# Kernel tuning notes

Measured on AMD Instinct MI355X. Metric: run time of the kernel, lower is better.

Reference implementation:

```python
import jax, jax.numpy as jnp
import numpy as np

EPS = 1e-5

def _layernorm(x, gamma, beta):
    # LayerNormalization over last axis (channels), epsilon=1e-5
    mu = jnp.mean(x, axis=-1, keepdims=True)
    var = jnp.var(x, axis=-1, keepdims=True)
    return (x - mu) * jax.lax.rsqrt(var + EPS) * gamma + beta

def setup_inputs() -> dict:
    key = jax.random.key(0)
    ks = jax.random.split(key, 6)
    B, H, W, C = 8, 64, 64, 256
    std = 0.1  # NIN init_scale
    return {
        "x": jax.random.normal(ks[0], (B, H, W, C), dtype=jnp.float32),
        "ln_gamma": jnp.ones((C,), dtype=jnp.float32),
        "ln_beta": jnp.zeros((C,), dtype=jnp.float32),
        "wq": jax.random.normal(ks[1], (C, C), dtype=jnp.float32) * std,
        "bq": jnp.zeros((C,), dtype=jnp.float32),
        "wk": jax.random.normal(ks[2], (C, C), dtype=jnp.float32) * std,
        "bk": jnp.zeros((C,), dtype=jnp.float32),
        "wv": jax.random.normal(ks[3], (C, C), dtype=jnp.float32) * std,
        "bv": jnp.zeros((C,), dtype=jnp.float32),
        "wo": jax.random.normal(ks[4], (C, C), dtype=jnp.float32) * std,
        "bo": jnp.zeros((C,), dtype=jnp.float32),
    }

def reference(x, ln_gamma, ln_beta, wq, bq, wk, bk, wv, bv, wo, bo):
    B, H, W, C = x.shape
    h = _layernorm(x, ln_gamma, ln_beta)
    # 1x1 convs == per-pixel channel matmuls
    q = jnp.einsum('bhwc,cd->bhwd', h, wq) + bq
    k = jnp.einsum('bhwc,cd->bhwd', h, wk) + bk
    v = jnp.einsum('bhwc,cd->bhwd', h, wv) + bv
    scale = jnp.float32(C) ** -0.5
    # dense spatial attention over all H*W tokens
    w = jnp.einsum('bhwc,bijc->bhwij', q, k) * scale  # [B,H,W,H,W]
    w = jax.nn.softmax(w.reshape(B, H, W, H * W), axis=-1).reshape(B, H, W, H, W)
    h = jnp.einsum('bhwij,bijc->bhwc', w, v)
    h = jnp.einsum('bhwc,cd->bhwd', h, wo) + bo
    return x + h
```

## Files before the change

### kernel.cpp

```cpp
#include <hip/hip_runtime.h>
#include <stdint.h>

#define NB    8
#define NTOK  4096
#define TOK   32768
#define CDIM  256
#define BQ    128
#define BK    64
#define NT    (NTOK / BK)

#define KPITCH 264
#define VPITCH 68
#define KTILE_SH (BK * KPITCH)
#define VTILE_SH (CDIM * VPITCH)
#define KCH   33
#define VCH   34
#define TOTCH (KCH + VCH)

typedef __attribute__((ext_vector_type(8))) short bf16x8;
typedef __attribute__((ext_vector_type(4))) float f32x4;

#define SSCALE 0.09016844f

static __device__ __forceinline__ unsigned short f2bf(float f) {
    union { float f; unsigned u; } v; v.f = f;
    unsigned r = v.u + 0x7fffu + ((v.u >> 16) & 1u);
    return (unsigned short)(r >> 16);
}

static __device__ __forceinline__ void dma16(const unsigned short* g, unsigned short* l) {
    __builtin_amdgcn_global_load_lds(
        (const __attribute__((address_space(1))) unsigned int*)g,
        (__attribute__((address_space(3))) unsigned int*)l,
        16, 0, 0);
}

__global__ __launch_bounds__(256) void prep_kernel(
        const float* __restrict__ x,
        const float* __restrict__ gamma,
        const float* __restrict__ beta,
        const float* __restrict__ w0, const float* __restrict__ w1,
        const float* __restrict__ w2, const float* __restrict__ w3,
        unsigned short* __restrict__ h_bf,
        unsigned short* __restrict__ wt) {
    int bx = blockIdx.x;
    if (bx >= TOK / 4) {
        int id = bx - TOK / 4;
        int m = id >> 8, dd = id & 255;
        const float* src = (m == 0) ? w0 : (m == 1) ? w1 : (m == 2) ? w2 : w3;
        wt[m * (CDIM * CDIM) + dd * CDIM + threadIdx.x] = f2bf(src[threadIdx.x * CDIM + dd]);
        return;
    }
    int w = threadIdx.x >> 6;
    int lane = threadIdx.x & 63;
    int token = bx * 4 + w;
    const float4 xv = ((const float4*)(x + (size_t)token * CDIM))[lane];
    float s = xv.x + xv.y + xv.z + xv.w;
    #pragma unroll
    for (int off = 1; off < 64; off <<= 1) s += __shfl_xor(s, off, 64);
    float mean = s * (1.0f / 256.0f);
    float d0 = xv.x - mean, d1 = xv.y - mean, d2 = xv.z - mean, d3 = xv.w - mean;
    float ss = d0 * d0 + d1 * d1 + d2 * d2 + d3 * d3;
    #pragma unroll
    for (int off = 1; off < 64; off <<= 1) ss += __shfl_xor(ss, off, 64);
    float rstd = rsqrtf(ss * (1.0f / 256.0f) + 1e-5f);
    float4 g = ((const float4*)gamma)[lane];
    float4 b = ((const float4*)beta)[lane];
    ushort4 o;
    o.x = f2bf(d0 * rstd * g.x + b.x);
    o.y = f2bf(d1 * rstd * g.y + b.y);
    o.z = f2bf(d2 * rstd * g.z + b.z);
    o.w = f2bf(d3 * rstd * g.w + b.w);
    ((ushort4*)(h_bf + (size_t)token * CDIM))[lane] = o;
}

__global__ __launch_bounds__(128) void qkv_kernel(
        const unsigned short* __restrict__ h_bf,
        const unsigned short* __restrict__ wts,
        const float* __restrict__ bq,
        const float* __restrict__ bk,
        const float* __restrict__ bv,
        unsigned short* __restrict__ q_bf,
        unsigned short* __restrict__ k2,
        unsigned short* __restrict__ vt2) {
    __shared__ unsigned short VT[64][VPITCH];
    int tid = threadIdx.x;
    int w = tid >> 6, lane = tid & 63, quad = lane >> 4, l16 = lane & 15;
    int blk = blockIdx.x;
    int gy = blockIdx.y;
    int nt0 = gy * 4;
    int tok_base = blk * 64 + w * 32;

    bf16x8 afr[2][8];
    #pragma unroll
    for (int s = 0; s < 2; ++s)
        #pragma unroll
        for (int kk = 0; kk < 8; ++kk)
            afr[s][kk] = *(const bf16x8*)(h_bf + (size_t)(tok_base + s * 16 + l16) * CDIM + kk * 32 + quad * 8);

    {
        const unsigned short* wq_t = wts;
        #pragma unroll
        for (int ntl = 0; ntl < 4; ++ntl) {
            int nt = nt0 + ntl;
            f32x4 acc0 = {0.f, 0.f, 0.f, 0.f};
            f32x4 acc1 = {0.f, 0.f, 0.f, 0.f};
            #pragma unroll
            for (int kk = 0; kk < 8; ++kk) {
                bf16x8 bfr = *(const bf16x8*)(wq_t + (size_t)(nt * 16 + l16) * CDIM + kk * 32 + quad * 8);
                acc0 = __builtin_amdgcn_mfma_f32_16x16x32_bf16(afr[0][kk], bfr, acc0, 0, 0, 0);
                acc1 = __builtin_amdgcn_mfma_f32_16x16x32_bf16(afr[1][kk], bfr, acc1, 0, 0, 0);
            }
            int d = nt * 16 + l16;
            float bb = bq[d];
            #pragma unroll
            for (int r = 0; r < 4; ++r) {
                q_bf[(size_t)(tok_base + quad * 4 + r) * CDIM + d]      = f2bf((acc0[r] + bb) * SSCALE);
                q_bf[(size_t)(tok_base + 16 + quad * 4 + r) * CDIM + d] = f2bf((acc1[r] + bb) * SSCALE);
            }
        }
    }
    {
        const unsigned short* wk_t = wts + CDIM * CDIM;
        unsigned short* kdst = k2 + (size_t)blk * KTILE_SH;
        int row0 = w * 32 + quad * 4;
        #pragma unroll
        for (int ntl = 0; ntl < 4; ++ntl) {
            int nt = nt0 + ntl;
            f32x4 acc0 = {0.f, 0.f, 0.f, 0.f};
            f32x4 acc1 = {0.f, 0.f, 0.f, 0.f};
            #pragma unroll
            for (int kk = 0; kk < 8; ++kk) {
                bf16x8 bfr = *(const bf16x8*)(wk_t + (size_t)(nt * 16 + l16) * CDIM + kk * 32 + quad * 8);
                acc0 = __builtin_amdgcn_mfma_f32_16x16x32_bf16(afr[0][kk], bfr, acc0, 0, 0, 0);
                acc1 = __builtin_amdgcn_mfma_f32_16x16x32_bf16(afr[1][kk], bfr, acc1, 0, 0, 0);
            }
            int d = nt * 16 + l16;
            float bb = bk[d];
            #pragma unroll
            for (int r = 0; r < 4; ++r) {
                kdst[(size_t)(row0 + r) * KPITCH + d]      = f2bf(acc0[r] + bb);
                kdst[(size_t)(row0 + 16 + r) * KPITCH + d] = f2bf(acc1[r] + bb);
            }
        }
    }
    {
        const unsigned short* wv_t = wts + 2 * CDIM * CDIM;
        int col0 = w * 32 + quad * 4;
        #pragma unroll
        for (int ntl = 0; ntl < 4; ++ntl) {
            int nt = nt0 + ntl;
            f32x4 acc0 = {0.f, 0.f, 0.f, 0.f};
            f32x4 acc1 = {0.f, 0.f, 0.f, 0.f};
            #pragma unroll
            for (int kk = 0; kk < 8; ++kk) {
                bf16x8 bfr = *(const bf16x8*)(wv_t + (size_t)(nt * 16 + l16) * CDIM + kk * 32 + quad * 8);
                acc0 = __builtin_amdgcn_mfma_f32_16x16x32_bf16(afr[0][kk], bfr, acc0, 0, 0, 0);
                acc1 = __builtin_amdgcn_mfma_f32_16x16x32_bf16(afr[1][kk], bfr, acc1, 0, 0, 0);
            }
            int d = nt * 16 + l16;
            float bb = bv[d];
            int dl = ntl * 16 + l16;
            #pragma unroll
            for (int r = 0; r < 4; ++r) {
                VT[dl][col0 + r]      = f2bf(acc0[r] + bb);
                VT[dl][col0 + 16 + r] = f2bf(acc1[r] + bb);
            }
        }
    }
    __syncthreads();
    const uint4* src = (const uint4*)(&VT[0][0]);
    uint4* dst = (uint4*)(vt2 + (size_t)blk * VTILE_SH + (size_t)gy * 64 * VPITCH);
    #pragma unroll
    for (int i = 0; i < 4; ++i)
        dst[i * 128 + tid] = src[i * 128 + tid];
    if (tid < 32) dst[512 + tid] = src[512 + tid];
}

#define DMA_TILE(KS, VS, ktn)                                                        \
    {                                                                                \
        const unsigned short* gk = k2 + (size_t)(b * NT + (ktn)) * KTILE_SH;         \
        const unsigned short* gv = vt2 + (size_t)(b * NT + (ktn)) * VTILE_SH;        \
        for (int c = w; c < TOTCH; c += 8) {                                         \
            if (c < KCH) dma16(gk + c * 512 + lane * 8, &KS[0][0] + c * 512);        \
            else dma16(gv + (c - KCH) * 512 + lane * 8, &VS[0][0] + (c - KCH) * 512);\
        }                                                                            \
    }

#define COMPUTE_TILE(KS, VS)                                                         \
    {                                                                                \
        f32x4 sfr[2][2];                                                             \
        _Pragma("unroll")                                                            \
        for (int nt = 0; nt < 2; ++nt) {                                             \
            f32x4 a0 = {0.f, 0.f, 0.f, 0.f};                                         \
            f32x4 a1 = {0.f, 0.f, 0.f, 0.f};                                         \
            _Pragma("unroll")                                                        \
            for (int kk = 0; kk < 8; ++kk) {                                         \
                bf16x8 kb = *(const bf16x8*)(&KS[kh * 32 + nt * 16 + l16][kk * 32 + quad * 8]); \
                a0 = __builtin_amdgcn_mfma_f32_16x16x32_bf16(qfr[0][kk], kb, a0, 0, 0, 0);      \
                a1 = __builtin_amdgcn_mfma_f32_16x16x32_bf16(qfr[1][kk], kb, a1, 0, 0, 0);      \
            }                                                                        \
            sfr[0][nt] = a0; sfr[1][nt] = a1;                                        \
        }                                                                            \
        _Pragma("unroll")                                                            \
        for (int s = 0; s < 2; ++s)                                                  \
            _Pragma("unroll")                                                        \
            for (int nt = 0; nt < 2; ++nt)                                           \
                _Pragma("unroll")                                                    \
                for (int r = 0; r < 4; ++r) {                                        \
                    float p = exp2f(sfr[s][nt][r]);                                  \
                    lacc[s][r] += p;                                                 \
                    Pl[wq * 32 + s * 16 + quad * 4 + r][kh * 32 + nt * 16 + l16] =   \
                        (unsigned short)(__float_as_uint(p) >> 16);                  \
                }                                                                    \
        bf16x8 pfr0 = *(const bf16x8*)(&Pl[wq * 32 + l16][kh * 32 + quad * 8]);      \
        bf16x8 pfr1 = *(const bf16x8*)(&Pl[wq * 32 + 16 + l16][kh * 32 + quad * 8]); \
        _Pragma("unroll")                                                            \
        for (int nt2 = 0; nt2 < 16; ++nt2) {                                         \
            bf16x8 vb = *(const bf16x8*)(&VS[nt2 * 16 + l16][kh * 32 + quad * 8]);   \
            O[0][nt2] = __builtin_amdgcn_mfma_f32_16x16x32_bf16(pfr0, vb, O[0][nt2], 0, 0, 0);  \
            O[1][nt2] = __builtin_amdgcn_mfma_f32_16x16x32_bf16(pfr1, vb, O[1][nt2], 0, 0, 0);  \
        }                                                                            \
    }

__global__ __launch_bounds__(512, 2) void flash_kernel(
        const unsigned short* __restrict__ q_bf,
        const unsigned short* __restrict__ k2,
        const unsigned short* __restrict__ vt2,
        unsigned short* __restrict__ attn) {
    __shared__ unsigned short Ks0[BK][KPITCH];
    __shared__ unsigned short Ks1[BK][KPITCH];
    __shared__ unsigned short Vs0[CDIM][VPITCH];
    __shared__ unsigned short Vs1[CDIM][VPITCH];
    __shared__ unsigned short Pl[BQ][VPITCH];

    int tid = threadIdx.x;
    int w = tid >> 6, lane = tid & 63, quad = lane >> 4, l16 = lane & 15;
    int kh = w >> 2;
    int wq = w & 3;
    int bid = blockIdx.x;
    int b = bid & 7;
    int qtile = bid >> 3;
    int qrow = qtile * BQ + wq * 32;
    const size_t bbase = (size_t)b * NTOK * CDIM;

    bf16x8 qfr[2][8];
    #pragma unroll
    for (int s = 0; s < 2; ++s)
        #pragma unroll
        for (int kk = 0; kk < 8; ++kk)
            qfr[s][kk] = *(const bf16x8*)(q_bf + bbase + (size_t)(qrow + s * 16 + l16) * CDIM + kk * 32 + quad * 8);

    f32x4 O[2][16];
    #pragma unroll
    for (int s = 0; s < 2; ++s)
        #pragma unroll
        for (int i = 0; i < 16; ++i) O[s][i] = (f32x4){0.f, 0.f, 0.f, 0.f};
    float lacc[2][4] = {{0.f, 0.f, 0.f, 0.f}, {0.f, 0.f, 0.f, 0.f}};

    DMA_TILE(Ks0, Vs0, 0);
    __syncthreads();

    for (int kt2 = 0; kt2 < NT; kt2 += 2) {
        DMA_TILE(Ks1, Vs1, kt2 + 1);
        COMPUTE_TILE(Ks0, Vs0);
        __syncthreads();
        if (kt2 + 2 < NT) DMA_TILE(Ks0, Vs0, kt2 + 2);
        COMPUTE_TILE(Ks1, Vs1);
        __syncthreads();
    }

    float* sO = (wq == 0) ? (float*)&Ks0[0][0] : (wq == 1) ? (float*)&Ks1[0][0]
              : (wq == 2) ? (float*)&Vs0[0][0] : (float*)&Vs1[0][0];
    float* sL = (float*)&Pl[0][0] + wq * 512;

    if (kh == 1) {
        #pragma unroll
        for (int s = 0; s < 2; ++s) {
            #pragma unroll
            for (int nt2 = 0; nt2 < 16; ++nt2)
                #pragma unroll
                for (int r = 0; r < 4; ++r)
                    sO[((s * 16 + nt2) * 4 + r) * 64 + lane] = O[s][nt2][r];
            #pragma unroll
            for (int r = 0; r < 4; ++r)
                sL[(s * 4 + r) * 64 + lane] = lacc[s][r];
        }
    }
    __syncthreads();
    if (kh == 0) {
        float linv[2][4];
        #pragma unroll
        for (int s = 0; s < 2; ++s)
            #pragma unroll
            for (int r = 0; r < 4; ++r) {
                float ls = lacc[s][r] + sL[(s * 4 + r) * 64 + lane];
                #pragma unroll
                for (int off = 1; off < 16; off <<= 1)
                    ls += __shfl_xor(ls, off, 64);
                linv[s][r] = 1.0f / ls;
            }
        #pragma unroll
        for (int s = 0; s < 2; ++s)
            #pragma unroll
            for (int nt2 = 0; nt2 < 16; ++nt2) {
                int d = nt2 * 16 + l16;
                #pragma unroll
                for (int r = 0; r < 4; ++r) {
                    float val = (O[s][nt2][r] + sO[((s * 16 + nt2) * 4 + r) * 64 + lane]) * linv[s][r];
                    attn[bbase + (size_t)(qrow + s * 16 + quad * 4 + r) * CDIM + d] = f2bf(val);
                }
            }
    }
}

__global__ __launch_bounds__(128) void oproj_kernel(
        const unsigned short* __restrict__ attn,
        const unsigned short* __restrict__ wo_t,
        const float* __restrict__ bo,
        const float* __restrict__ x,
        float* __restrict__ out) {
    int w = threadIdx.x >> 6, lane = threadIdx.x & 63;
    int quad = lane >> 4, l16 = lane & 15;
    int tok_base = blockIdx.x * 64 + w * 32;
    int nt0 = blockIdx.y * 8;

    bf16x8 afr[2][8];
    #pragma unroll
    for (int s = 0; s < 2; ++s)
        #pragma unroll
        for (int kk = 0; kk < 8; ++kk)
            afr[s][kk] = *(const bf16x8*)(attn + (size_t)(tok_base + s * 16 + l16) * CDIM + kk * 32 + quad * 8);

    #pragma unroll
    for (int ntl = 0; ntl < 8; ++ntl) {
        int nt = nt0 + ntl;
        f32x4 acc0 = {0.f, 0.f, 0.f, 0.f};
        f32x4 acc1 = {0.f, 0.f, 0.f, 0.f};
        #pragma unroll
        for (int kk = 0; kk < 8; ++kk) {
            bf16x8 bfr = *(const bf16x8*)(wo_t + (size_t)(nt * 16 + l16) * CDIM + kk * 32 + quad * 8);
            acc0 = __builtin_amdgcn_mfma_f32_16x16x32_bf16(afr[0][kk], bfr, acc0, 0, 0, 0);
            acc1 = __builtin_amdgcn_mfma_f32_16x16x32_bf16(afr[1][kk], bfr, acc1, 0, 0, 0);
        }
        int d = nt * 16 + l16;
        float bb = bo[d];
        #pragma unroll
        for (int r = 0; r < 4; ++r) {
            size_t idx0 = (size_t)(tok_base + quad * 4 + r) * CDIM + d;
            size_t idx1 = (size_t)(tok_base + 16 + quad * 4 + r) * CDIM + d;
            out[idx0] = x[idx0] + acc0[r] + bb;
            out[idx1] = x[idx1] + acc1[r] + bb;
        }
    }
}

extern "C" void kernel_launch(void* const* d_in, const int* in_sizes, int n_in,
                              void* d_out, int out_size, void* d_ws, size_t ws_size,
                              hipStream_t stream) {
    const float* x     = (const float*)d_in[0];
    const float* gamma = (const float*)d_in[1];
    const float* beta  = (const float*)d_in[2];
    const float* wq    = (const float*)d_in[3];
    const float* bq    = (const float*)d_in[4];
    const float* wk    = (const float*)d_in[5];
    const float* bk    = (const float*)d_in[6];
    const float* wv    = (const float*)d_in[7];
    const float* bv    = (const float*)d_in[8];
    const float* wo    = (const float*)d_in[9];
    const float* bo    = (const float*)d_in[10];
    float* out = (float*)d_out;

    char* ws = (char*)d_ws;
    unsigned short* h_bf = (unsigned short*)(ws);
    unsigned short* q_bf = (unsigned short*)(ws + 16777216);
    unsigned short* k2   = (unsigned short*)(ws + 33554432);
    unsigned short* vt2  = (unsigned short*)(ws + 50855936);
    unsigned short* wt   = (unsigned short*)(ws + 68681728);
    unsigned short* attn = h_bf;

    prep_kernel<<<TOK / 4 + 1024, 256, 0, stream>>>(x, gamma, beta, wq, wk, wv, wo, h_bf, wt);
    qkv_kernel<<<dim3(TOK / 64, 4), 128, 0, stream>>>(h_bf, wt, bq, bk, bv, q_bf, k2, vt2);
    flash_kernel<<<(NTOK / BQ) * NB, 512, 0, stream>>>(q_bf, k2, vt2, attn);
    oproj_kernel<<<dim3(TOK / 64, 2), 128, 0, stream>>>(attn, wt + 3 * (CDIM * CDIM), bo, x, out);
}
```

Baseline: 362.3 us.

## Keep softmax probabilities in registers by transposing QK MFMA and permuting V layout

Swaps the MFMA operands in the QK^T product so each lane holds the scores for a single query row across consecutive key positions. Those probabilities are then packed straight into the bf16x8 A-fragment for the PV MFMA, with no round trip through an LDS P buffer. The V transpose store is permuted to match the resulting key ordering, and the row-sum bookkeeping and final normalization shuffles are reworked for the new lane mapping. This removes per-tile LDS writes and reads for P, at the cost of a different reduction pattern and correctness that depends on the V permutation matching exactly.

```diff
diff --git a/kernel.cpp b/kernel.cpp
--- a/kernel.cpp
+++ b/kernel.cpp
@@ -146,7 +146,6 @@
     }
     {
         const unsigned short* wv_t = wts + 2 * CDIM * CDIM;
-        int col0 = w * 32 + quad * 4;
         #pragma unroll
         for (int ntl = 0; ntl < 4; ++ntl) {
             int nt = nt0 + ntl;
@@ -163,8 +162,8 @@
             int dl = ntl * 16 + l16;
             #pragma unroll
             for (int r = 0; r < 4; ++r) {
-                VT[dl][col0 + r]      = f2bf(acc0[r] + bb);
-                VT[dl][col0 + 16 + r] = f2bf(acc1[r] + bb);
+                VT[dl][w * 32 + quad * 8 + r]     = f2bf(acc0[r] + bb);
+                VT[dl][w * 32 + quad * 8 + 4 + r] = f2bf(acc1[r] + bb);
             }
         }
     }
@@ -197,24 +196,29 @@
             _Pragma("unroll")                                                        \
             for (int kk = 0; kk < 8; ++kk) {                                         \
                 bf16x8 kb = *(const bf16x8*)(&KS[kh * 32 + nt * 16 + l16][kk * 32 + quad * 8]); \
-                a0 = __builtin_amdgcn_mfma_f32_16x16x32_bf16(qfr[0][kk], kb, a0, 0, 0, 0);      \
-                a1 = __builtin_amdgcn_mfma_f32_16x16x32_bf16(qfr[1][kk], kb, a1, 0, 0, 0);      \
+                a0 = __builtin_amdgcn_mfma_f32_16x16x32_bf16(kb, qfr[0][kk], a0, 0, 0, 0);      \
+                a1 = __builtin_amdgcn_mfma_f32_16x16x32_bf16(kb, qfr[1][kk], a1, 0, 0, 0);      \
             }                                                                        \
             sfr[0][nt] = a0; sfr[1][nt] = a1;                                        \
         }                                                                            \
+        int4 pwv[2];                                                                 \
         _Pragma("unroll")                                                            \
-        for (int s = 0; s < 2; ++s)                                                  \
+        for (int s = 0; s < 2; ++s) {                                                \
+            unsigned pw[4];                                                          \
             _Pragma("unroll")                                                        \
             for (int nt = 0; nt < 2; ++nt)                                           \
                 _Pragma("unroll")                                                    \
-                for (int r = 0; r < 4; ++r) {                                        \
-                    float p = exp2f(sfr[s][nt][r]);                                  \
-                    lacc[s][r] += p;                                                 \
-                    Pl[wq * 32 + s * 16 + quad * 4 + r][kh * 32 + nt * 16 + l16] =   \
-                        (unsigned short)(__float_as_uint(p) >> 16);                  \
+                for (int h = 0; h < 2; ++h) {                                        \
+                    float plo = exp2f(sfr[s][nt][2 * h]);                            \
+                    float phi = exp2f(sfr[s][nt][2 * h + 1]);                        \
+                    lacc[s] += plo + phi;                                            \
+                    pw[nt * 2 + h] = (__float_as_uint(plo) >> 16)                    \
+                                   | (__float_as_uint(phi) & 0xffff0000u);           \
                 }                                                                    \
-        bf16x8 pfr0 = *(const bf16x8*)(&Pl[wq * 32 + l16][kh * 32 + quad * 8]);      \
-        bf16x8 pfr1 = *(const bf16x8*)(&Pl[wq * 32 + 16 + l16][kh * 32 + quad * 8]); \
+            pwv[s] = make_int4(pw[0], pw[1], pw[2], pw[3]);                          \
+        }                                                                            \
+        bf16x8 pfr0 = *(bf16x8*)&pwv[0];                                             \
+        bf16x8 pfr1 = *(bf16x8*)&pwv[1];                                             \
         _Pragma("unroll")                                                            \
         for (int nt2 = 0; nt2 < 16; ++nt2) {                                         \
             bf16x8 vb = *(const bf16x8*)(&VS[nt2 * 16 + l16][kh * 32 + quad * 8]);   \
@@ -232,7 +236,7 @@
     __shared__ unsigned short Ks1[BK][KPITCH];
     __shared__ unsigned short Vs0[CDIM][VPITCH];
     __shared__ unsigned short Vs1[CDIM][VPITCH];
-    __shared__ unsigned short Pl[BQ][VPITCH];
+    __shared__ float sLbuf[512];
 
     int tid = threadIdx.x;
     int w = tid >> 6, lane = tid & 63, quad = lane >> 4, l16 = lane & 15;
@@ -256,7 +260,7 @@
     for (int s = 0; s < 2; ++s)
         #pragma unroll
         for (int i = 0; i < 16; ++i) O[s][i] = (f32x4){0.f, 0.f, 0.f, 0.f};
-    float lacc[2][4] = {{0.f, 0.f, 0.f, 0.f}, {0.f, 0.f, 0.f, 0.f}};
+    float lacc[2] = {0.f, 0.f};
 
     DMA_TILE(Ks0, Vs0, 0);
     __syncthreads();
@@ -272,7 +276,7 @@
 
     float* sO = (wq == 0) ? (float*)&Ks0[0][0] : (wq == 1) ? (float*)&Ks1[0][0]
               : (wq == 2) ? (float*)&Vs0[0][0] : (float*)&Vs1[0][0];
-    float* sL = (float*)&Pl[0][0] + wq * 512;
+    float* sL = sLbuf + wq * 128;
 
     if (kh == 1) {
         #pragma unroll
@@ -282,24 +286,22 @@
                 #pragma unroll
                 for (int r = 0; r < 4; ++r)
                     sO[((s * 16 + nt2) * 4 + r) * 64 + lane] = O[s][nt2][r];
-            #pragma unroll
-            for (int r = 0; r < 4; ++r)
-                sL[(s * 4 + r) * 64 + lane] = lacc[s][r];
+            sL[s * 64 + lane] = lacc[s];
         }
     }
     __syncthreads();
     if (kh == 0) {
-        float linv[2][4];
-        #pragma unroll
-        for (int s = 0; s < 2; ++s)
-            #pragma unroll
-            for (int r = 0; r < 4; ++r) {
-                float ls = lacc[s][r] + sL[(s * 4 + r) * 64 + lane];
-                #pragma unroll
-                for (int off = 1; off < 16; off <<= 1)
-                    ls += __shfl_xor(ls, off, 64);
-                linv[s][r] = 1.0f / ls;
-            }
+        float lr[2][4];
+        #pragma unroll
+        for (int s = 0; s < 2; ++s) {
+            float ls = lacc[s] + sL[s * 64 + lane];
+            ls += __shfl_xor(ls, 16, 64);
+            ls += __shfl_xor(ls, 32, 64);
+            float li = 1.0f / ls;
+            #pragma unroll
+            for (int r = 0; r < 4; ++r)
+                lr[s][r] = __shfl(li, quad * 4 + r, 64);
+        }
         #pragma unroll
         for (int s = 0; s < 2; ++s)
             #pragma unroll
@@ -307,7 +309,7 @@
                 int d = nt2 * 16 + l16;
                 #pragma unroll
                 for (int r = 0; r < 4; ++r) {
-                    float val = (O[s][nt2][r] + sO[((s * 16 + nt2) * 4 + r) * 64 + lane]) * linv[s][r];
+                    float val = (O[s][nt2][r] + sO[((s * 16 + nt2) * 4 + r) * 64 + lane]) * lr[s][r];
                     attn[bbase + (size_t)(qrow + s * 16 + quad * 4 + r) * CDIM + d] = f2bf(val);
                 }
             }
```

After: 363.4 us. No clear change (+0.3%).
